# Optimization experiments

Hardware: AMD Instinct MI355X
Metric: run time of the kernel (lower is better)

## Reference

```python
import jax, jax.numpy as jnp
import numpy as np

B, T, U, D = 8, 200, 50, 512
INNER, VOCAB = 640, 1024


def setup_inputs() -> dict:
    key = jax.random.key(0)
    k1, k2, k3, k4 = jax.random.split(key, 4)
    enc_outputs = jax.random.normal(k1, (B, T, D), dtype=jnp.float32)
    dec_outputs = jax.random.normal(k2, (B, U, D), dtype=jnp.float32)
    # Dense(inner_dim, activation='tanh') params
    W1 = jax.random.normal(k3, (D, INNER), dtype=jnp.float32) / np.sqrt(D)
    b1 = jnp.zeros((INNER,), dtype=jnp.float32)
    # Dense(vocab_size) params
    W2 = jax.random.normal(k4, (INNER, VOCAB), dtype=jnp.float32) / np.sqrt(INNER)
    b2 = jnp.zeros((VOCAB,), dtype=jnp.float32)
    return {"enc_outputs": enc_outputs, "dec_outputs": dec_outputs,
            "W1": W1, "b1": b1, "W2": W2, "b2": b2}


def reference(enc_outputs, dec_outputs, W1, b1, W2, b2):
    # joint_inputs: (B, T, U, D) via broadcast add, exactly as the TF module
    joint = enc_outputs[:, :, None, :] + dec_outputs[:, None, :, :]
    hidden = jnp.tanh(jnp.einsum('btud,dh->btuh', joint, W1) + b1)  # (B,T,U,INNER)
    logits = jnp.einsum('btuh,hv->btuv', hidden, W2) + b2            # (B,T,U,VOCAB)
    return logits
```

## Files before the change

kernel.cpp:

```cpp
#include <hip/hip_runtime.h>
#include <hip/hip_bf16.h>
#include <stdint.h>

namespace {

constexpr int B = 8, T = 200, U = 50, D = 512, INNER = 640, VOCAB = 1024;
constexpr int M_TOTAL = B * T * U;
constexpr int ROWS_E = B * T;
constexpr int ROWS_D = B * U;
constexpr int ROWS_ED = ROWS_E + ROWS_D;
constexpr int BM = 128, BN = 512;
constexpr int CK = 128;

typedef __bf16 bf16x8 __attribute__((ext_vector_type(8)));
typedef float  f32x4  __attribute__((ext_vector_type(4)));
typedef unsigned short u16;
typedef unsigned int   u32;

constexpr size_t ED_BYTES = (size_t)ROWS_ED * INNER * 4;

__device__ __forceinline__ u16 f2bf(float f) {
  uint32_t u = __float_as_uint(f);
  uint32_t rounding = 0x7FFFu + ((u >> 16) & 1u);
  return (u16)((u + rounding) >> 16);
}

__device__ __forceinline__ float fast_tanh(float x) {
  float e = __expf(2.0f * x);
  float r = __builtin_amdgcn_rcpf(e + 1.0f);
  return 1.0f - 2.0f * r;
}

__global__ __launch_bounds__(320) void k_prep(const float* __restrict__ enc,
                                              const float* __restrict__ dec,
                                              const float* __restrict__ W1,
                                              const float* __restrict__ b1,
                                              const float* __restrict__ W2,
                                              float* __restrict__ ED,
                                              u16* __restrict__ W2B) {
  if (blockIdx.x >= 500) {
    const int idx = (blockIdx.x - 500) * 320 + threadIdx.x;
    const int lane = idx & 63;
    const int f = idx >> 6;
    const int ks = f >> 6;
    const int nf = f & 63;
    const int n = nf * 16 + (lane & 15);
    const int k = ks * 32 + (lane >> 4) * 8;
    u16 v[8];
#pragma unroll
    for (int j = 0; j < 8; ++j)
      v[j] = f2bf(W2[(size_t)(k + j) * VOCAB + n]);
    uint64_t lo = (uint64_t)v[0] | ((uint64_t)v[1] << 16) |
                  ((uint64_t)v[2] << 32) | ((uint64_t)v[3] << 48);
    uint64_t hi = (uint64_t)v[4] | ((uint64_t)v[5] << 16) |
                  ((uint64_t)v[6] << 32) | ((uint64_t)v[7] << 48);
    uint64_t* dst = reinterpret_cast<uint64_t*>(W2B + (size_t)idx * 8);
    dst[0] = lo;
    dst[1] = hi;
    return;
  }

  __shared__ float rows[4 * D];
  const int r0 = blockIdx.x * 4;
  const bool is_enc = (r0 < ROWS_E);
  const float* src = is_enc ? (enc + (size_t)r0 * D)
                            : (dec + (size_t)(r0 - ROWS_E) * D);
  for (int i = threadIdx.x; i < 4 * D; i += 320) rows[i] = src[i];
  __syncthreads();

  const int c0 = threadIdx.x, c1 = threadIdx.x + 320;
  float acc[4][2];
  const float bias0 = is_enc ? b1[c0] : 0.f;
  const float bias1 = is_enc ? b1[c1] : 0.f;
#pragma unroll
  for (int r = 0; r < 4; ++r) { acc[r][0] = bias0; acc[r][1] = bias1; }

  for (int d = 0; d < D; d += 8) {
    f32x4 rv[4][2];
#pragma unroll
    for (int r = 0; r < 4; ++r) {
      rv[r][0] = *reinterpret_cast<const f32x4*>(&rows[r * D + d]);
      rv[r][1] = *reinterpret_cast<const f32x4*>(&rows[r * D + d + 4]);
    }
#pragma unroll
    for (int dd = 0; dd < 8; ++dd) {
      const float w0 = W1[(size_t)(d + dd) * INNER + c0];
      const float w1 = W1[(size_t)(d + dd) * INNER + c1];
#pragma unroll
      for (int r = 0; r < 4; ++r) {
        const float x = rv[r][dd >> 2][dd & 3];
        acc[r][0] = fmaf(x, w0, acc[r][0]);
        acc[r][1] = fmaf(x, w1, acc[r][1]);
      }
    }
  }
#pragma unroll
  for (int r = 0; r < 4; ++r) {
    ED[(size_t)(r0 + r) * INNER + c0] = acc[r][0];
    ED[(size_t)(r0 + r) * INNER + c1] = acc[r][1];
  }
}

__global__ __launch_bounds__(1024, 4) void k_main(const float* __restrict__ ED,
                                                  const u16* __restrict__ W2B,
                                                  const float* __restrict__ b2,
                                                  float* __restrict__ out) {
  __shared__ u16 At[2][BM * CK];
  const int tid = threadIdx.x;
  const int m0 = blockIdx.x * BM;
  const int n0 = blockIdx.y * BN;

  const int row = tid >> 3;
  const int g   = tid & 7;
  const int m = m0 + row;
  const int bb = m / (T * U);
  const int rem = m - bb * (T * U);
  const int tt = rem / U;
  const int uu = rem - tt * U;
  const float* Erow = ED + (size_t)(bb * T + tt) * INNER;
  const float* Drow = ED + (size_t)(ROWS_E + bb * U + uu) * INNER;
  const int wb0 = (((row >> 4) * 4 + (g >> 1)) << 10) +
                  (((g & 1) * 2) * 16 + (row & 15)) * 16;

  auto tanh_chunk = [&](int c, int bufsel) __attribute__((always_inline)) {
    char* dst = reinterpret_cast<char*>(At[bufsel]);
#pragma unroll
    for (int h = 0; h < 2; ++h) {
      const int kk = c * CK + g * 16 + h * 8;
      const f32x4 e0 = *reinterpret_cast<const f32x4*>(Erow + kk);
      const f32x4 e1 = *reinterpret_cast<const f32x4*>(Erow + kk + 4);
      const f32x4 d0 = *reinterpret_cast<const f32x4*>(Drow + kk);
      const f32x4 d1 = *reinterpret_cast<const f32x4*>(Drow + kk + 4);
      int4 pk;
      pk.x = (int)((u32)f2bf(fast_tanh(e0[0] + d0[0])) |
                   ((u32)f2bf(fast_tanh(e0[1] + d0[1])) << 16));
      pk.y = (int)((u32)f2bf(fast_tanh(e0[2] + d0[2])) |
                   ((u32)f2bf(fast_tanh(e0[3] + d0[3])) << 16));
      pk.z = (int)((u32)f2bf(fast_tanh(e1[0] + d1[0])) |
                   ((u32)f2bf(fast_tanh(e1[1] + d1[1])) << 16));
      pk.w = (int)((u32)f2bf(fast_tanh(e1[2] + d1[2])) |
                   ((u32)f2bf(fast_tanh(e1[3] + d1[3])) << 16));
      *reinterpret_cast<int4*>(dst + wb0 + h * 256) = pk;
    }
  };

  const int lane = tid & 63;
  const int w    = tid >> 6;
  const int wr = w >> 3, wc = w & 7;
  const int llo = lane & 15, lhi = lane >> 4;
  const u16* Bp = W2B + ((size_t)((n0 >> 4) + wc * 4) << 9) + lane * 8;
  const int albase = lane * 16;

  f32x4 acc[4][4];
#pragma unroll
  for (int mi = 0; mi < 4; ++mi)
#pragma unroll
    for (int ni = 0; ni < 4; ++ni) acc[mi][ni] = (f32x4){0.f, 0.f, 0.f, 0.f};

  tanh_chunk(0, 0);
  __syncthreads();

  for (int c = 0; c < 5; ++c) {
    const char* asrc = reinterpret_cast<const char*>(At[c & 1]);
    if (c < 4) tanh_chunk(c + 1, (c + 1) & 1);

#pragma unroll
    for (int kq = 0; kq < 4; ++kq) {
      bf16x8 a[4], bfr[4];
#pragma unroll
      for (int ni = 0; ni < 4; ++ni)
        bfr[ni] = *reinterpret_cast<const bf16x8*>(
            Bp + ((size_t)((c * 4 + kq) * 64 + ni) << 9));
#pragma unroll
      for (int mi = 0; mi < 4; ++mi)
        a[mi] = *reinterpret_cast<const bf16x8*>(
            asrc + ((((wr * 4 + mi) << 2) + kq) << 10) + albase);
#pragma unroll
      for (int mi = 0; mi < 4; ++mi)
#pragma unroll
        for (int ni = 0; ni < 4; ++ni)
          acc[mi][ni] = __builtin_amdgcn_mfma_f32_16x16x32_bf16(a[mi], bfr[ni], acc[mi][ni], 0, 0, 0);
    }
    __syncthreads();
  }

  float b2v[4];
#pragma unroll
  for (int ni = 0; ni < 4; ++ni) b2v[ni] = b2[n0 + wc * 64 + ni * 16 + llo];

#pragma unroll
  for (int mi = 0; mi < 4; ++mi) {
#pragma unroll
    for (int q = 0; q < 4; ++q) {
      const int r = m0 + wr * 64 + mi * 16 + lhi * 4 + q;
      float* orow = out + (size_t)r * VOCAB + n0 + wc * 64 + llo;
#pragma unroll
      for (int ni = 0; ni < 4; ++ni)
        __builtin_nontemporal_store(acc[mi][ni][q] + b2v[ni], orow + ni * 16);
    }
  }
}

}

extern "C" void kernel_launch(void* const* d_in, const int* in_sizes, int n_in,
                              void* d_out, int out_size, void* d_ws, size_t ws_size,
                              hipStream_t stream) {
  const float* enc = (const float*)d_in[0];
  const float* dec = (const float*)d_in[1];
  const float* W1  = (const float*)d_in[2];
  const float* b1  = (const float*)d_in[3];
  const float* W2  = (const float*)d_in[4];
  const float* b2  = (const float*)d_in[5];
  float* out = (float*)d_out;

  float* ED  = (float*)d_ws;
  u16*   W2B = (u16*)((char*)d_ws + ED_BYTES);

  hipLaunchKernelGGL(k_prep, dim3(756), dim3(320), 0, stream,
                     enc, dec, W1, b1, W2, ED, W2B);
  hipLaunchKernelGGL(k_main, dim3(M_TOTAL / BM, VOCAB / BN), dim3(1024), 0, stream,
                     ED, W2B, b2, out);
}
```

Before: 214.1 us.

## Use 8-wave blocks with 128x64 per-wave tiles and prefetched W2 fragments

Shrinks the main GEMM block from 16 to 8 waves, so each wave computes all 128 rows times 64 columns (8x4 MFMA tiles) instead of a 64x64 tile. Each B fragment is reused across twice as many MFMAs, which halves global B traffic per output. The next k-step's W2 fragments are register-prefetched before the current MFMAs issue. The tanh staging is reorganised so each wave writes its own 16-row slab directly in MFMA layout. In exchange, accumulators double to 128 floats per thread, raising register pressure and lowering occupancy to two blocks of 512 threads.

```diff
diff --git a/kernel.cpp b/kernel.cpp
--- a/kernel.cpp
+++ b/kernel.cpp
@@ -101,36 +101,39 @@
   }
 }
 
-__global__ __launch_bounds__(1024, 4) void k_main(const float* __restrict__ ED,
-                                                  const u16* __restrict__ W2B,
-                                                  const float* __restrict__ b2,
-                                                  float* __restrict__ out) {
+__global__ __launch_bounds__(512, 2) void k_main(const float* __restrict__ ED,
+                                                 const u16* __restrict__ W2B,
+                                                 const float* __restrict__ b2,
+                                                 float* __restrict__ out) {
   __shared__ u16 At[2][BM * CK];
   const int tid = threadIdx.x;
   const int m0 = blockIdx.x * BM;
   const int n0 = blockIdx.y * BN;
 
-  const int row = tid >> 3;
-  const int g   = tid & 7;
-  const int m = m0 + row;
+  const int lane = tid & 63;
+  const int wv   = tid >> 6;
+  const int llo  = lane & 15;
+  const int lhi  = lane >> 4;
+
+  const int trow = wv * 16 + llo;
+  const int m = m0 + trow;
   const int bb = m / (T * U);
   const int rem = m - bb * (T * U);
   const int tt = rem / U;
   const int uu = rem - tt * U;
   const float* Erow = ED + (size_t)(bb * T + tt) * INNER;
   const float* Drow = ED + (size_t)(ROWS_E + bb * U + uu) * INNER;
-  const int wb0 = (((row >> 4) * 4 + (g >> 1)) << 10) +
-                  (((g & 1) * 2) * 16 + (row & 15)) * 16;
+  const int klo = lhi * 8;
 
   auto tanh_chunk = [&](int c, int bufsel) __attribute__((always_inline)) {
-    char* dst = reinterpret_cast<char*>(At[bufsel]);
-#pragma unroll
-    for (int h = 0; h < 2; ++h) {
-      const int kk = c * CK + g * 16 + h * 8;
-      const f32x4 e0 = *reinterpret_cast<const f32x4*>(Erow + kk);
-      const f32x4 e1 = *reinterpret_cast<const f32x4*>(Erow + kk + 4);
-      const f32x4 d0 = *reinterpret_cast<const f32x4*>(Drow + kk);
-      const f32x4 d1 = *reinterpret_cast<const f32x4*>(Drow + kk + 4);
+    char* dst = reinterpret_cast<char*>(At[bufsel]) + (wv << 12) + lane * 16;
+#pragma unroll
+    for (int kq = 0; kq < 4; ++kq) {
+      const int k = c * CK + kq * 32 + klo;
+      const f32x4 e0 = *reinterpret_cast<const f32x4*>(Erow + k);
+      const f32x4 e1 = *reinterpret_cast<const f32x4*>(Erow + k + 4);
+      const f32x4 d0 = *reinterpret_cast<const f32x4*>(Drow + k);
+      const f32x4 d1 = *reinterpret_cast<const f32x4*>(Drow + k + 4);
       int4 pk;
       pk.x = (int)((u32)f2bf(fast_tanh(e0[0] + d0[0])) |
                    ((u32)f2bf(fast_tanh(e0[1] + d0[1])) << 16));
@@ -140,24 +143,24 @@
                    ((u32)f2bf(fast_tanh(e1[1] + d1[1])) << 16));
       pk.w = (int)((u32)f2bf(fast_tanh(e1[2] + d1[2])) |
                    ((u32)f2bf(fast_tanh(e1[3] + d1[3])) << 16));
-      *reinterpret_cast<int4*>(dst + wb0 + h * 256) = pk;
+      *reinterpret_cast<int4*>(dst + (kq << 10)) = pk;
     }
   };
 
-  const int lane = tid & 63;
-  const int w    = tid >> 6;
-  const int wr = w >> 3, wc = w & 7;
-  const int llo = lane & 15, lhi = lane >> 4;
-  const u16* Bp = W2B + ((size_t)((n0 >> 4) + wc * 4) << 9) + lane * 8;
+  const u16* Bp = W2B + ((size_t)((n0 >> 4) + wv * 4) << 9) + lane * 8;
   const int albase = lane * 16;
 
-  f32x4 acc[4][4];
-#pragma unroll
-  for (int mi = 0; mi < 4; ++mi)
+  f32x4 acc[8][4];
+#pragma unroll
+  for (int mi = 0; mi < 8; ++mi)
 #pragma unroll
     for (int ni = 0; ni < 4; ++ni) acc[mi][ni] = (f32x4){0.f, 0.f, 0.f, 0.f};
 
   tanh_chunk(0, 0);
+  bf16x8 bcur[4], bnext[4];
+#pragma unroll
+  for (int ni = 0; ni < 4; ++ni)
+    bcur[ni] = *reinterpret_cast<const bf16x8*>(Bp + ((size_t)ni << 9));
   __syncthreads();
 
   for (int c = 0; c < 5; ++c) {
@@ -166,34 +169,41 @@
 
 #pragma unroll
     for (int kq = 0; kq < 4; ++kq) {
-      bf16x8 a[4], bfr[4];
-#pragma unroll
-      for (int ni = 0; ni < 4; ++ni)
-        bfr[ni] = *reinterpret_cast<const bf16x8*>(
-            Bp + ((size_t)((c * 4 + kq) * 64 + ni) << 9));
-#pragma unroll
-      for (int mi = 0; mi < 4; ++mi)
+      const int ks = c * 4 + kq;
+      if (ks < 19) {
+#pragma unroll
+        for (int ni = 0; ni < 4; ++ni)
+          bnext[ni] = *reinterpret_cast<const bf16x8*>(
+              Bp + ((size_t)((ks + 1) * 64 + ni) << 9));
+      }
+      bf16x8 a[8];
+#pragma unroll
+      for (int mi = 0; mi < 8; ++mi)
         a[mi] = *reinterpret_cast<const bf16x8*>(
-            asrc + ((((wr * 4 + mi) << 2) + kq) << 10) + albase);
-#pragma unroll
-      for (int mi = 0; mi < 4; ++mi)
+            asrc + (((mi << 2) + kq) << 10) + albase);
+#pragma unroll
+      for (int mi = 0; mi < 8; ++mi)
 #pragma unroll
         for (int ni = 0; ni < 4; ++ni)
-          acc[mi][ni] = __builtin_amdgcn_mfma_f32_16x16x32_bf16(a[mi], bfr[ni], acc[mi][ni], 0, 0, 0);
+          acc[mi][ni] = __builtin_amdgcn_mfma_f32_16x16x32_bf16(a[mi], bcur[ni], acc[mi][ni], 0, 0, 0);
+      if (ks < 19) {
+#pragma unroll
+        for (int ni = 0; ni < 4; ++ni) bcur[ni] = bnext[ni];
+      }
     }
     __syncthreads();
   }
 
   float b2v[4];
 #pragma unroll
-  for (int ni = 0; ni < 4; ++ni) b2v[ni] = b2[n0 + wc * 64 + ni * 16 + llo];
-
-#pragma unroll
-  for (int mi = 0; mi < 4; ++mi) {
+  for (int ni = 0; ni < 4; ++ni) b2v[ni] = b2[n0 + wv * 64 + ni * 16 + llo];
+
+#pragma unroll
+  for (int mi = 0; mi < 8; ++mi) {
 #pragma unroll
     for (int q = 0; q < 4; ++q) {
-      const int r = m0 + wr * 64 + mi * 16 + lhi * 4 + q;
-      float* orow = out + (size_t)r * VOCAB + n0 + wc * 64 + llo;
+      const int r = m0 + mi * 16 + lhi * 4 + q;
+      float* orow = out + (size_t)r * VOCAB + n0 + wv * 64 + llo;
 #pragma unroll
       for (int ni = 0; ni < 4; ++ni)
         __builtin_nontemporal_store(acc[mi][ni][q] + b2v[ni], orow + ni * 16);
@@ -219,6 +229,6 @@
 
   hipLaunchKernelGGL(k_prep, dim3(756), dim3(320), 0, stream,
                      enc, dec, W1, b1, W2, ED, W2B);
-  hipLaunchKernelGGL(k_main, dim3(M_TOTAL / BM, VOCAB / BN), dim3(1024), 0, stream,
+  hipLaunchKernelGGL(k_main, dim3(M_TOTAL / BM, VOCAB / BN), dim3(512), 0, stream,
                      ED, W2B, b2, out);
 }
```

After: 219.5 us. +2.5%, slower.
